# Performance work log

Measured on AMD Instinct MI355X. Metric: run time of the kernel, lower is better.

Reference implementation:

```python
import jax, jax.numpy as jnp
import numpy as np


def _bce_with_logits(x, t):
    # numerically-stable binary_cross_entropy_with_logits, reduction='none'
    return jnp.maximum(x, 0.0) - x * t + jnp.log1p(jnp.exp(-jnp.abs(x)))


def _compute_weights(targets):
    """Replicates the scipy.ndimage.label / sum_labels weighting.

    4-connected component labeling (scipy default structure) via iterative
    min-label propagation, then per-pixel component area, then
    1 / (sqrt(area) + 1) with zeros replaced by the global mean of the
    nonzero sqrt-areas.
    """
    B, H, W = targets.shape
    HW = H * W  # sentinel label for background
    fg = targets > 0
    base = jnp.arange(HW, dtype=jnp.int32).reshape(1, H, W)
    lab0 = jnp.where(fg, base, HW).astype(jnp.int32)

    def cond(state):
        return state[1]

    def body(state):
        lab, _ = state
        p = jnp.pad(lab, ((0, 0), (1, 1), (1, 1)), constant_values=HW)
        nb = jnp.minimum(jnp.minimum(p[:, :-2, 1:-1], p[:, 2:, 1:-1]),
                         jnp.minimum(p[:, 1:-1, :-2], p[:, 1:-1, 2:]))
        new = jnp.where(fg, jnp.minimum(lab, nb), HW)
        return new, jnp.any(new != lab)

    lab, _ = jax.lax.while_loop(cond, body, (lab0, jnp.array(True)))

    def per_sample_area(lab_i, fg_i):
        sizes = jax.ops.segment_sum(fg_i.ravel().astype(jnp.float32),
                                    lab_i.ravel(), num_segments=HW + 1)
        return sizes[lab_i]  # [H, W] area of each pixel's component

    area = jax.vmap(per_sample_area)(lab, fg)
    area = jnp.where(fg, area, 0.0)

    w = jnp.sqrt(area)
    nz = w > 0
    # global (whole-tensor) mean of nonzero sqrt-areas, as in the torch code
    mean_nz = jnp.sum(jnp.where(nz, w, 0.0)) / jnp.maximum(
        jnp.sum(nz.astype(jnp.float32)), 1.0)
    w_filled = jnp.where(nz, w, mean_nz)
    return 1.0 / (w_filled + 1.0)


def setup_inputs() -> dict:
    key = jax.random.key(0)
    k1, k2 = jax.random.split(key)
    B, H, W = 32, 512, 512
    inputs = jax.random.normal(k1, (B, H, W), dtype=jnp.float32)
    # sparse binary mask (subcritical density -> small blobs, like vessels)
    targets = (jax.random.uniform(k2, (B, H, W)) < 0.3).astype(jnp.float32)
    return {"inputs": inputs, "targets": targets}


def reference(inputs, targets):
    weights = _compute_weights(targets)
    bce = _bce_with_logits(inputs, targets)
    return jnp.mean(weights * bce)
```

## Files before the change

### kernel.cpp

```cpp
#include <hip/hip_runtime.h>
#include <math.h>

static constexpr int IMG_W  = 512;
static constexpr int IMG_PX = 512 * 512;
static constexpr int NIMG   = 32;
static constexpr int TILE_W = 64;
static constexpr int TILE_H = 32;
static constexpr int TPX    = IMG_W / TILE_W;
static constexpr int TPY    = IMG_W / TILE_H;
static constexpr int TILES_PER_IMG = TPX * TPY;
static constexpr int FUSED_BLOCKS  = NIMG * TILES_PER_IMG;
static constexpr int DEF_BLOCKS    = 512;
static constexpr int MIG_BLOCKS    = 512;
static constexpr int PART_TOTAL    = FUSED_BLOCKS + DEF_BLOCKS;
static constexpr int LCAP    = 128;
static constexpr int FLAGBIT = 1 << 30;
static constexpr int CNTMASK = FLAGBIT - 1;
static constexpr int TPIX    = TILE_W * TILE_H;


__device__ __forceinline__ int find_root_g(const int* L, int x) {
    int p = L[x];
    while (p != x) { x = p; p = L[x]; }
    return x;
}

__device__ __forceinline__ void merge_g(int* L, int a, int b) {
    while (true) {
        a = find_root_g(L, a);
        b = find_root_g(L, b);
        if (a == b) return;
        if (a < b) { int t = a; a = b; b = t; }
        int old = atomicMin(&L[a], b);
        if (old == a) return;
        a = old;
    }
}


__device__ __forceinline__ int find_root_l(volatile int* sl, int x) {
    int p = sl[x];
    while (p != x) { x = p; p = sl[x]; }
    return p;
}

__device__ __forceinline__ void merge_l(int* sl, int a, int b) {
    while (true) {
        a = find_root_l(sl, a);
        b = find_root_l(sl, b);
        if (a == b) return;
        if (a < b) { int t = a; a = b; b = t; }
        int old = atomicMin(&sl[a], b);
        if (old == a) return;
        a = old;
    }
}

__device__ __forceinline__ void block_reduce_write(float s_fg, float s_bg,
                                                   float s_sq, float s_n,
                                                   double4* __restrict__ part,
                                                   int slot) {
    for (int o = 32; o > 0; o >>= 1) {
        s_fg += __shfl_down(s_fg, o, 64);
        s_bg += __shfl_down(s_bg, o, 64);
        s_sq += __shfl_down(s_sq, o, 64);
        s_n  += __shfl_down(s_n,  o, 64);
    }
    __shared__ double4 wsum[4];
    int wave = threadIdx.x >> 6;
    if ((threadIdx.x & 63) == 0)
        wsum[wave] = make_double4((double)s_fg, (double)s_bg, (double)s_sq, (double)s_n);
    __syncthreads();
    if (threadIdx.x == 0) {
        double4 b = wsum[0];
        for (int wv = 1; wv < 4; wv++) {
            b.x += wsum[wv].x; b.y += wsum[wv].y;
            b.z += wsum[wv].z; b.w += wsum[wv].w;
        }
        part[slot] = b;
    }
}

__device__ __forceinline__ float bce0_fast(float xx) {
    return fmaxf(xx, 0.f) + __logf(1.f + __expf(-fabsf(xx)));
}


__global__ __launch_bounds__(256) void ccl_fused(const float* __restrict__ t,
                                                 const float* __restrict__ x,
                                                 int* __restrict__ L,
                                                 int* __restrict__ area,
                                                 int4* __restrict__ list,
                                                 int* __restrict__ blockcount,
                                                 double4* __restrict__ part,
                                                 int* __restrict__ done) {
    __shared__ int   sl[TPIX];
    __shared__ int   cnt[TPIX];
    __shared__ float fsum[TPIX];
    __shared__ unsigned long long rowmask[TILE_H];
    __shared__ int   lcount;

    int blk = blockIdx.x;
    int b   = blk / TILES_PER_IMG;
    int tid = blk % TILES_PER_IMG;
    int tY  = tid / TPX, tX = tid % TPX;
    int k   = threadIdx.x;
    int col = k & 63, wv = k >> 6;
    int base = b * IMG_PX + (tY * TILE_H) * IMG_W + tX * TILE_W;

    if (k == 0) lcount = 0;
    if (blk == 0 && k == 0) *done = 0;

    float xr[8];
#pragma unroll
    for (int s = 0; s < 8; s++) {
        int row = wv * 8 + s;
        int jj  = row * TILE_W + col;
        int g   = base + row * IMG_W + col;
        float tv = t[g];
        xr[s] = x[g];
        bool fg = (tv != 0.f);
        unsigned long long mask = __ballot(fg);
        if (col == 0) rowmask[row] = mask;
        int lab = -1;
        if (fg) {
            unsigned long long startm = mask & ~(mask << 1);
            unsigned long long low = (col == 63) ? ~0ULL : ((1ULL << (col + 1)) - 1ULL);
            lab = row * TILE_W + (63 - __clzll(startm & low));
        }
        sl[jj]   = lab;
        cnt[jj]  = 0;
        fsum[jj] = 0.f;
    }
    __syncthreads();

#pragma unroll
    for (int s = 0; s < 8; s++) {
        int row = wv * 8 + s;
        if (row == 0) continue;
        unsigned long long both = rowmask[row] & rowmask[row - 1];
        unsigned long long pairstart = both & ~(both << 1);
        if ((pairstart >> col) & 1ULL)
            merge_l(sl, row * TILE_W + col, (row - 1) * TILE_W + col);
    }
    __syncthreads();

#pragma unroll
    for (int s = 0; s < 8; s++) {
        int row = wv * 8 + s;
        unsigned long long mask = rowmask[row];
        unsigned long long startm = mask & ~(mask << 1);
        if ((startm >> col) & 1ULL) {
            unsigned long long inv = ~(mask >> col);
            int len = inv ? (__ffsll((long long)inv) - 1) : (64 - col);
            int jj = row * TILE_W + col;
            int r = find_root_l(sl, jj);
            sl[jj] = r;
            atomicAdd(&cnt[r], len);
        }
    }
    __syncthreads();

    {
        int r = -1, c = -1;
        if      (k < 64)  { r = 0;          c = k;          }
        else if (k < 128) { r = TILE_H - 1; c = k - 64;     }
        else if (k < 160) { r = k - 128;    c = 0;          }
        else if (k < 192) { r = k - 160;    c = TILE_W - 1; }
        if (r >= 0) {
            int jj = r * TILE_W + c;
            int g  = base + r * IMG_W + c;
            int s0 = sl[jj];
            if (s0 >= 0) {
                int root = sl[s0];
                atomicOr(&cnt[root], FLAGBIT);
                L[g] = base + (root >> 6) * IMG_W + (root & 63);
            } else {
                L[g] = -1;
            }
        }
    }
    __syncthreads();

    float s_fg = 0.f, s_bg = 0.f, s_sq = 0.f, s_n = 0.f;
#pragma unroll
    for (int s = 0; s < 8; s++) {
        int row = wv * 8 + s;
        int jj  = row * TILE_W + col;
        float xx = xr[s];
        float b0 = bce0_fast(xx);
        int s0 = sl[jj];
        if (s0 < 0) {
            s_bg += b0;
        } else {
            int root = sl[s0];
            int cc = cnt[root];
            float bce1 = b0 - xx;
            if (cc & FLAGBIT) {
                atomicAdd(&fsum[root], bce1);
            } else {
                float w = sqrtf((float)cc);
                s_fg += bce1 / (w + 1.f);
                s_sq += w;
                s_n  += 1.f;
            }
        }
    }
    __syncthreads();

    int4* mylist = list + blk * LCAP;
#pragma unroll
    for (int s = 0; s < 8; s++) {
        int jj = (wv * 8 + s) * TILE_W + col;
        if (sl[jj] == jj && (cnt[jj] & FLAGBIT)) {
            int slot = atomicAdd(&lcount, 1);
            int g = base + (jj >> 6) * IMG_W + (jj & 63);
            int c = cnt[jj] & CNTMASK;
            if (slot < LCAP)
                mylist[slot] = make_int4(g, __float_as_int(fsum[jj]), c, 0);
            area[g] = c;
            L[g]    = g;
        }
    }
    block_reduce_write(s_fg, s_bg, s_sq, s_n, part, blk);
    if (k == 0) blockcount[blk] = min(lcount, LCAP);
}

__global__ void ccl_border(int* __restrict__ L, int nEdges) {
    int e = blockIdx.x * blockDim.x + threadIdx.x;
    if (e >= nEdges) return;
    const int nV = (TPX - 1) * IMG_W;
    const int nH = (TPY - 1) * IMG_W;
    int perImg = nV + nH;
    int b = e / perImg;
    int v = e - b * perImg;
    int g, nbr;
    if (v < nV) {
        int bi = v / IMG_W;
        int y  = v - bi * IMG_W;
        int xx = TILE_W * (bi + 1);
        g = b * IMG_PX + y * IMG_W + xx;
        nbr = g - 1;
    } else {
        int v2 = v - nV;
        int bi = v2 / IMG_W;
        int xx = v2 - bi * IMG_W;
        int y  = TILE_H * (bi + 1);
        g = b * IMG_PX + y * IMG_W + xx;
        nbr = g - IMG_W;
    }
    if (L[g] >= 0 && L[nbr] >= 0) merge_g(L, g, nbr);
}

__global__ void fix_migrate(int* __restrict__ L, int* __restrict__ area,
                            const int4* __restrict__ list,
                            const int* __restrict__ blockcount) {
    const int nSlots = FUSED_BLOCKS * LCAP;
    int stride = gridDim.x * blockDim.x;
    for (int i = blockIdx.x * blockDim.x + threadIdx.x; i < nSlots; i += stride) {
        int blk  = i >> 7;
        int slot = i & (LCAP - 1);
        if (slot < blockcount[blk]) {
            int4 ent = list[i];
            int g = ent.x;
            int r = find_root_g(L, g);
            if (r != g) { atomicAdd(&area[r], ent.z); L[g] = r; }
        }
    }
}

__global__ __launch_bounds__(256) void deferred_final(const int4* __restrict__ list,
                                                      const int* __restrict__ blockcount,
                                                      const int* __restrict__ L,
                                                      const int* __restrict__ area,
                                                      double4* __restrict__ part,
                                                      int* __restrict__ done,
                                                      float* __restrict__ out,
                                                      int N) {
    const int nSlots = FUSED_BLOCKS * LCAP;
    float s_fg = 0.f, s_sq = 0.f, s_n = 0.f;
    int stride = gridDim.x * blockDim.x;
    for (int i = blockIdx.x * blockDim.x + threadIdx.x; i < nSlots; i += stride) {
        int blk  = i >> 7;
        int slot = i & (LCAP - 1);
        if (slot < blockcount[blk]) {
            int4 ent = list[i];
            int r = find_root_g(L, ent.x);
            float w = sqrtf((float)area[r]);
            float c = (float)ent.z;
            s_fg += __int_as_float(ent.y) / (w + 1.f);
            s_sq += c * w;
            s_n  += c;
        }
    }
    block_reduce_write(s_fg, 0.f, s_sq, s_n, part, FUSED_BLOCKS + blockIdx.x);

    __shared__ int amlast;
    if (threadIdx.x == 0) {
        __threadfence();
        int old = atomicAdd(done, 1);
        amlast = (old == (int)gridDim.x - 1);
    }
    __syncthreads();
    if (!amlast) return;
    __threadfence();

    double fg = 0.0, bg = 0.0, sq = 0.0, nn = 0.0;
    for (int i = threadIdx.x; i < PART_TOTAL; i += blockDim.x) {
        double4 p = part[i];
        fg += p.x; bg += p.y; sq += p.z; nn += p.w;
    }
    for (int o = 32; o > 0; o >>= 1) {
        fg += __shfl_down(fg, o, 64);
        bg += __shfl_down(bg, o, 64);
        sq += __shfl_down(sq, o, 64);
        nn += __shfl_down(nn, o, 64);
    }
    __shared__ double4 f2[4];
    int wave = threadIdx.x >> 6;
    if ((threadIdx.x & 63) == 0) f2[wave] = make_double4(fg, bg, sq, nn);
    __syncthreads();
    if (threadIdx.x == 0) {
        double4 bb = f2[0];
        for (int wv = 1; wv < 4; wv++) {
            bb.x += f2[wv].x; bb.y += f2[wv].y;
            bb.z += f2[wv].z; bb.w += f2[wv].w;
        }
        double mean_nz = bb.z / fmax(bb.w, 1.0);
        double loss = (bb.x + bb.y / (mean_nz + 1.0)) / (double)N;
        out[0] = (float)loss;
    }
}


extern "C" void kernel_launch(void* const* d_in, const int* in_sizes, int n_in,
                              void* d_out, int out_size, void* d_ws, size_t ws_size,
                              hipStream_t stream) {
    const float* x = (const float*)d_in[0];
    const float* t = (const float*)d_in[1];
    float* out = (float*)d_out;
    int N = in_sizes[0];

    int* L          = (int*)d_ws;
    int* area       = L + N;
    double4* part   = (double4*)(area + N);
    int* blockcount = (int*)(part + PART_TOTAL);
    int* done       = blockcount + FUSED_BLOCKS;
    int4* list      = (int4*)(done + 4);

    ccl_fused<<<FUSED_BLOCKS, 256, 0, stream>>>(t, x, L, area, list, blockcount,
                                                part, done);
    const int nEdges = NIMG * ((TPX - 1) + (TPY - 1)) * IMG_W;
    ccl_border<<<(nEdges + 255) / 256, 256, 0, stream>>>(L, nEdges);
    fix_migrate<<<MIG_BLOCKS, 256, 0, stream>>>(L, area, list, blockcount);
    deferred_final<<<DEF_BLOCKS, 256, 0, stream>>>(list, blockcount, L, area,
                                                   part, done, out, N);
}
```

Baseline: 177.7 us.

## Replace border scan kernel with compact seam list built in fused CCL kernel

During the fused tile pass, each block checks whether its edge pixels have a foreground neighbour across the tile seam. Blocks that own the bottom and right edges append each such pixel pair to a per-block seam list. A new seam_merge kernel runs union-find merges only on those recorded pairs, replacing the kernel that visited every seam pixel. Roots are now flagged for migration only when they actually touch a foreground neighbour, which shrinks the list fix_migrate has to process. The cost is an extra global read of the neighbouring target value per edge pixel, plus a fixed-capacity seam buffer that still has to be scanned slot by slot.

```diff
diff --git a/kernel.cpp b/kernel.cpp
--- a/kernel.cpp
+++ b/kernel.cpp
@@ -10,10 +10,12 @@
 static constexpr int TPY    = IMG_W / TILE_H;
 static constexpr int TILES_PER_IMG = TPX * TPY;
 static constexpr int FUSED_BLOCKS  = NIMG * TILES_PER_IMG;
+static constexpr int SEAM_BLOCKS   = 512;
+static constexpr int MIG_BLOCKS    = 512;
 static constexpr int DEF_BLOCKS    = 512;
-static constexpr int MIG_BLOCKS    = 512;
 static constexpr int PART_TOTAL    = FUSED_BLOCKS + DEF_BLOCKS;
 static constexpr int LCAP    = 128;
+static constexpr int SCAP    = 128;
 static constexpr int FLAGBIT = 1 << 30;
 static constexpr int CNTMASK = FLAGBIT - 1;
 static constexpr int TPIX    = TILE_W * TILE_H;
@@ -92,13 +94,15 @@
                                                  int* __restrict__ area,
                                                  int4* __restrict__ list,
                                                  int* __restrict__ blockcount,
+                                                 int2* __restrict__ seams,
+                                                 int* __restrict__ seamcount,
                                                  double4* __restrict__ part,
                                                  int* __restrict__ done) {
     __shared__ int   sl[TPIX];
     __shared__ int   cnt[TPIX];
     __shared__ float fsum[TPIX];
     __shared__ unsigned long long rowmask[TILE_H];
-    __shared__ int   lcount;
+    __shared__ int   lcount, scount;
 
     int blk = blockIdx.x;
     int b   = blk / TILES_PER_IMG;
@@ -108,7 +112,7 @@
     int col = k & 63, wv = k >> 6;
     int base = b * IMG_PX + (tY * TILE_H) * IMG_W + tX * TILE_W;
 
-    if (k == 0) lcount = 0;
+    if (k == 0) { lcount = 0; scount = 0; }
     if (blk == 0 && k == 0) *done = 0;
 
     float xr[8];
@@ -162,21 +166,25 @@
     __syncthreads();
 
     {
-        int r = -1, c = -1;
-        if      (k < 64)  { r = 0;          c = k;          }
-        else if (k < 128) { r = TILE_H - 1; c = k - 64;     }
-        else if (k < 160) { r = k - 128;    c = 0;          }
-        else if (k < 192) { r = k - 160;    c = TILE_W - 1; }
+        int r = -1, c = 0, dg = 0; bool owner = false;
+        if      (k < 64)  { r = 0;          c = k;        dg = (tY > 0)       ? -IMG_W : 0; }
+        else if (k < 128) { r = TILE_H - 1; c = k - 64;   dg = (tY < TPY - 1) ?  IMG_W : 0; owner = true; }
+        else if (k < 160) { r = k - 128;    c = 0;        dg = (tX > 0)       ? -1     : 0; }
+        else if (k < 192) { r = k - 160;    c = TILE_W-1; dg = (tX < TPX - 1) ?  1     : 0; owner = true; }
         if (r >= 0) {
             int jj = r * TILE_W + c;
-            int g  = base + r * IMG_W + c;
             int s0 = sl[jj];
             if (s0 >= 0) {
                 int root = sl[s0];
-                atomicOr(&cnt[root], FLAGBIT);
+                int g = base + r * IMG_W + c;
                 L[g] = base + (root >> 6) * IMG_W + (root & 63);
-            } else {
-                L[g] = -1;
+                if (dg != 0 && t[g + dg] != 0.f) {
+                    atomicOr(&cnt[root], FLAGBIT);
+                    if (owner) {
+                        int s = atomicAdd(&scount, 1);
+                        if (s < SCAP) seams[blk * SCAP + s] = make_int2(g, g + dg);
+                    }
+                }
             }
         }
     }
@@ -223,38 +231,28 @@
         }
     }
     block_reduce_write(s_fg, s_bg, s_sq, s_n, part, blk);
-    if (k == 0) blockcount[blk] = min(lcount, LCAP);
-}
-
-__global__ void ccl_border(int* __restrict__ L, int nEdges) {
-    int e = blockIdx.x * blockDim.x + threadIdx.x;
-    if (e >= nEdges) return;
-    const int nV = (TPX - 1) * IMG_W;
-    const int nH = (TPY - 1) * IMG_W;
-    int perImg = nV + nH;
-    int b = e / perImg;
-    int v = e - b * perImg;
-    int g, nbr;
-    if (v < nV) {
-        int bi = v / IMG_W;
-        int y  = v - bi * IMG_W;
-        int xx = TILE_W * (bi + 1);
-        g = b * IMG_PX + y * IMG_W + xx;
-        nbr = g - 1;
-    } else {
-        int v2 = v - nV;
-        int bi = v2 / IMG_W;
-        int xx = v2 - bi * IMG_W;
-        int y  = TILE_H * (bi + 1);
-        g = b * IMG_PX + y * IMG_W + xx;
-        nbr = g - IMG_W;
-    }
-    if (L[g] >= 0 && L[nbr] >= 0) merge_g(L, g, nbr);
-}
-
-__global__ void fix_migrate(int* __restrict__ L, int* __restrict__ area,
-                            const int4* __restrict__ list,
-                            const int* __restrict__ blockcount) {
+    if (k == 0) { blockcount[blk] = min(lcount, LCAP); seamcount[blk] = min(scount, SCAP); }
+}
+
+__global__ __launch_bounds__(256) void seam_merge(int* __restrict__ L,
+                                                  const int2* __restrict__ seams,
+                                                  const int* __restrict__ seamcount) {
+    const int nSlots = FUSED_BLOCKS * SCAP;
+    int stride = gridDim.x * blockDim.x;
+    for (int i = blockIdx.x * blockDim.x + threadIdx.x; i < nSlots; i += stride) {
+        int blk  = i >> 7;
+        int slot = i & (SCAP - 1);
+        if (slot < seamcount[blk]) {
+            int2 p = seams[i];
+            merge_g(L, p.x, p.y);
+        }
+    }
+}
+
+__global__ __launch_bounds__(256) void fix_migrate(int* __restrict__ L,
+                                                   int* __restrict__ area,
+                                                   const int4* __restrict__ list,
+                                                   const int* __restrict__ blockcount) {
     const int nSlots = FUSED_BLOCKS * LCAP;
     int stride = gridDim.x * blockDim.x;
     for (int i = blockIdx.x * blockDim.x + threadIdx.x; i < nSlots; i += stride) {
@@ -345,13 +343,14 @@
     int* area       = L + N;
     double4* part   = (double4*)(area + N);
     int* blockcount = (int*)(part + PART_TOTAL);
-    int* done       = blockcount + FUSED_BLOCKS;
+    int* seamcount  = blockcount + FUSED_BLOCKS;
+    int* done       = seamcount + FUSED_BLOCKS;
     int4* list      = (int4*)(done + 4);
+    int2* seams     = (int2*)(list + FUSED_BLOCKS * LCAP);
 
     ccl_fused<<<FUSED_BLOCKS, 256, 0, stream>>>(t, x, L, area, list, blockcount,
-                                                part, done);
-    const int nEdges = NIMG * ((TPX - 1) + (TPY - 1)) * IMG_W;
-    ccl_border<<<(nEdges + 255) / 256, 256, 0, stream>>>(L, nEdges);
+                                                seams, seamcount, part, done);
+    seam_merge<<<SEAM_BLOCKS, 256, 0, stream>>>(L, seams, seamcount);
     fix_migrate<<<MIG_BLOCKS, 256, 0, stream>>>(L, area, list, blockcount);
     deferred_final<<<DEF_BLOCKS, 256, 0, stream>>>(list, blockcount, L, area,
                                                    part, done, out, N);
```

Result: no change. 177.5 us (-0.1%).
